# Kernel optimization log

Measured on AMD Instinct MI355X. Metric: run time of the kernel, lower is better.

The kernel has to match this reference:

```python
import jax, jax.numpy as jnp
import numpy as np

N = 20000      # nodes
E = 320000     # edges (before self-loops)
IN, HID, H, OUT = 256, 64, 8, 16
NEG_SLOPE = 0.2  # PyG GATConv default


def _gat_layer(x, src, dst, W, a_src, a_dst, b, heads, ch, concat):
    """One PyG-style GATConv (eval mode, self-loops already in src/dst).
    x: [N, F_in]; W: [F_in, heads*ch]; a_src/a_dst: [heads, ch]; b: bias."""
    n = x.shape[0]
    h = (x @ W).reshape(n, heads, ch)                      # [N, H, C]
    alpha_src = jnp.sum(h * a_src, axis=-1)                # [N, H]
    alpha_dst = jnp.sum(h * a_dst, axis=-1)                # [N, H]
    e = jax.nn.leaky_relu(alpha_src[src] + alpha_dst[dst], NEG_SLOPE)  # [Et, H]
    # segment softmax over incoming edges of each dst node (numerically stable)
    m = jax.ops.segment_max(e, dst, num_segments=n)
    m = jnp.where(jnp.isfinite(m), m, 0.0)
    ex = jnp.exp(e - m[dst])
    denom = jax.ops.segment_sum(ex, dst, num_segments=n)
    alpha = ex / jnp.maximum(denom[dst], 1e-16)            # [Et, H]
    # message = alpha * h[src], scatter-add to dst
    out = jax.ops.segment_sum(alpha[:, :, None] * h[src], dst, num_segments=n)  # [N,H,C]
    out = out.reshape(n, heads * ch) if concat else out.mean(axis=1)
    return out + b


def setup_inputs() -> dict:
    key = jax.random.key(0)
    ks = jax.random.split(key, 16)
    p = lambda k, shape, fan: (jax.random.normal(k, shape, jnp.float32) / np.float32(np.sqrt(fan)))
    return {
        "x": jax.random.normal(ks[0], (N, IN), jnp.float32),
        "edge_index": jax.random.randint(ks[1], (2, E), 0, N, dtype=jnp.int32),
        "W1": p(ks[2], (IN, H * HID), IN),
        "a_src1": p(ks[3], (H, HID), HID), "a_dst1": p(ks[4], (H, HID), HID),
        "b1": jnp.zeros((H * HID,), jnp.float32),
        "W2": p(ks[5], (H * HID, H * HID), H * HID),
        "a_src2": p(ks[6], (H, HID), HID), "a_dst2": p(ks[7], (H, HID), HID),
        "b2": jnp.zeros((H * HID,), jnp.float32),
        "W3": p(ks[8], (H * HID, OUT), H * HID),
        "a_src3": p(ks[9], (1, OUT), OUT), "a_dst3": p(ks[10], (1, OUT), OUT),
        "b3": jnp.zeros((OUT,), jnp.float32),
    }


def reference(x, edge_index, W1, a_src1, a_dst1, b1, W2, a_src2, a_dst2, b2,
              W3, a_src3, a_dst3, b3):
    # add self-loops once (PyG GATConv default add_self_loops=True)
    loops = jnp.arange(N, dtype=edge_index.dtype)
    src = jnp.concatenate([edge_index[0], loops])
    dst = jnp.concatenate([edge_index[1], loops])
    h = _gat_layer(x, src, dst, W1, a_src1, a_dst1, b1, H, HID, True)
    h = jax.nn.elu(h)
    h = _gat_layer(h, src, dst, W2, a_src2, a_dst2, b2, H, HID, True)
    h = jax.nn.elu(h)
    h = _gat_layer(h, src, dst, W3, a_src3, a_dst3, b3, 1, OUT, False)
    return jax.nn.log_softmax(h, axis=1)
```

## Files before the change

### kernel.cpp

```cpp
#include <hip/hip_runtime.h>
#include <hip/hip_fp8.h>

#define NEG_SLOPE 0.2f

typedef _Float16 f16x8 __attribute__((ext_vector_type(8)));
typedef float f32x4 __attribute__((ext_vector_type(4)));
typedef float f32x2 __attribute__((ext_vector_type(2)));

#if defined(__has_builtin)
#if __has_builtin(__builtin_amdgcn_cvt_pk_f32_fp8)
#define HAVE_PK_FP8 1
#endif
#endif

__device__ __forceinline__ float lrelu(float x){ return x >= 0.0f ? x : NEG_SLOPE * x; }
__device__ __forceinline__ float elu1(float x){ return x > 0.0f ? x : __expf(x) - 1.0f; }

__device__ __forceinline__ void gload_lds16(const _Float16* g, _Float16* l){
  __builtin_amdgcn_global_load_lds(
      (const __attribute__((address_space(1))) unsigned int*)g,
      (__attribute__((address_space(3))) unsigned int*)l, 16, 0, 0);
}

__device__ __forceinline__ float f8_to_f32(unsigned char b){
  __hip_fp8_e4m3 t; t.__x = (__hip_fp8_storage_t)b; return (float)t;
}

__device__ __forceinline__ void dq8(uint2 u, float* f){
#ifdef HAVE_PK_FP8
  f32x2 a = __builtin_amdgcn_cvt_pk_f32_fp8(u.x, false);
  f32x2 b = __builtin_amdgcn_cvt_pk_f32_fp8(u.x, true);
  f32x2 c = __builtin_amdgcn_cvt_pk_f32_fp8(u.y, false);
  f32x2 d = __builtin_amdgcn_cvt_pk_f32_fp8(u.y, true);
  f[0]=a[0]; f[1]=a[1]; f[2]=b[0]; f[3]=b[1];
  f[4]=c[0]; f[5]=c[1]; f[6]=d[0]; f[7]=d[1];
#else
  const unsigned char* p = (const unsigned char*)&u;
  #pragma unroll
  for (int j = 0; j < 8; ++j) f[j] = f8_to_f32(p[j]);
#endif
}

union H8U { uint4 u; _Float16 h[8]; };

__global__ __launch_bounds__(256) void prep_kernel(
    const float* __restrict__ x, _Float16* __restrict__ x16, int cvtb, int valid, int total,
    const float* __restrict__ W1, _Float16* __restrict__ W1T,
    const float* __restrict__ W2, _Float16* __restrict__ W2T,
    const int* __restrict__ dstp, int E, int N, int* __restrict__ counts)
{
  __shared__ float tile[32][33];
  int b = blockIdx.x;
  const int tid = threadIdx.x;
  if (b < cvtb){
    int i = (b * 256 + tid) * 8;
    if (i < total){
      H8U o;
      if (i + 8 <= valid){
        float4 v0 = *(const float4*)(x + i);
        float4 v1 = *(const float4*)(x + i + 4);
        o.h[0] = (_Float16)v0.x; o.h[1] = (_Float16)v0.y; o.h[2] = (_Float16)v0.z; o.h[3] = (_Float16)v0.w;
        o.h[4] = (_Float16)v1.x; o.h[5] = (_Float16)v1.y; o.h[6] = (_Float16)v1.z; o.h[7] = (_Float16)v1.w;
      } else {
        #pragma unroll
        for (int j = 0; j < 8; ++j) o.h[j] = (i + j < valid) ? (_Float16)x[i + j] : (_Float16)0.0f;
      }
      *(uint4*)(x16 + i) = o.u;
    }
    return;
  }
  b -= cvtb;
  if (b < 128 + 256){
    const float* W; _Float16* WT; int K, Nn, bb;
    if (b < 128){ W = W1; WT = W1T; K = 256; Nn = 512; bb = b; }
    else        { W = W2; WT = W2T; K = 512; Nn = 512; bb = b - 128; }
    const int nbk = K / 32;
    const int k0 = (bb % nbk) * 32, n0 = (bb / nbk) * 32;
    const int tx = tid & 31, ty = tid >> 5;
    for (int i = ty; i < 32; i += 8)
      tile[i][tx] = W[(size_t)(k0 + i) * Nn + n0 + tx];
    __syncthreads();
    for (int i = ty; i < 32; i += 8)
      WT[(size_t)(n0 + i) * K + k0 + tx] = (_Float16)tile[tx][i];
    return;
  }
  b -= 384;
  {
    int i = b * 256 + tid;
    if (i < E + N){
      int d = (i < E) ? dstp[i] : (i - E);
      atomicAdd(&counts[d], 1);
    }
  }
}

__global__ __launch_bounds__(256) void block_sum_kernel(const int* __restrict__ counts, int N, int* __restrict__ bsum){
  __shared__ int ws[4];
  const int lane = threadIdx.x & 63, wave = threadIdx.x >> 6;
  int i = blockIdx.x * 256 + threadIdx.x;
  int v = (i < N) ? counts[i] : 0;
  #pragma unroll
  for (int msk = 1; msk < 64; msk <<= 1) v += __shfl_xor(v, msk);
  if (lane == 0) ws[wave] = v;
  __syncthreads();
  if (threadIdx.x == 0) bsum[blockIdx.x] = ws[0] + ws[1] + ws[2] + ws[3];
}

__global__ __launch_bounds__(256) void scan_bsum_kernel(int* __restrict__ bsum, int nb, int* __restrict__ offsets, int N){
  __shared__ int tmp[256];
  const int t = threadIdx.x;
  int v = (t < nb) ? bsum[t] : 0;
  tmp[t] = v;
  __syncthreads();
  #pragma unroll
  for (int ofs = 1; ofs < 256; ofs <<= 1){
    int add = (t >= ofs) ? tmp[t - ofs] : 0;
    __syncthreads();
    tmp[t] += add;
    __syncthreads();
  }
  if (t < nb) bsum[t] = tmp[t] - v;
  if (t == nb - 1) offsets[N] = tmp[t];
}

__global__ __launch_bounds__(256) void scan_within_kernel(const int* __restrict__ counts, const int* __restrict__ bsum,
                                                          int* __restrict__ offsets, int N){
  __shared__ int wsum[4];
  const int lane = threadIdx.x & 63, wave = threadIdx.x >> 6;
  int i = blockIdx.x * 256 + threadIdx.x;
  int v = (i < N) ? counts[i] : 0;
  int sc = v;
  #pragma unroll
  for (int ofs = 1; ofs < 64; ofs <<= 1){
    int t = __shfl_up(sc, ofs);
    if (lane >= ofs) sc += t;
  }
  if (lane == 63) wsum[wave] = sc;
  __syncthreads();
  int woff = 0;
  #pragma unroll
  for (int w = 0; w < 4; ++w) if (w < wave) woff += wsum[w];
  if (i < N) offsets[i] = bsum[blockIdx.x] + woff + sc - v;
}

__global__ void fill_kernel(const int* __restrict__ src, const int* __restrict__ dst, int E, int N,
                            const int* __restrict__ offsets, int* __restrict__ cursor, int* __restrict__ csr_src){
  int i = blockIdx.x * blockDim.x + threadIdx.x;
  if (i < E + N){
    int s, d;
    if (i < E){ s = src[i]; d = dst[i]; } else { s = i - E; d = i - E; }
    int pos = atomicAdd(&cursor[d], 1);
    csr_src[offsets[d] + pos] = s;
  }
}

__global__ __launch_bounds__(256) void gemm_f16_mfma_q(
    const _Float16* __restrict__ A, const _Float16* __restrict__ BT,
    unsigned char* __restrict__ H8, float* __restrict__ SC,
    const float* __restrict__ a_src, const float* __restrict__ a_dst,
    float* __restrict__ AS, float* __restrict__ AD,
    int M, int Nn, int K)
{
  __shared__ _Float16 As[128 * 64];
  __shared__ _Float16 Bs[128 * 64];
  const int tid = threadIdx.x;
  const int lane = tid & 63;
  const int wave = tid >> 6;
  const int wr = wave >> 1, wc = wave & 1;
  const int row0 = blockIdx.x * 128;
  const int col0 = blockIdx.y * 128;
  const int r15 = lane & 15;
  const int kgrp = lane >> 4;
  const int head = 2 * blockIdx.y + wc;

  f32x4 acc[4][4];
  #pragma unroll
  for (int m = 0; m < 4; ++m)
    #pragma unroll
    for (int n = 0; n < 4; ++n)
      acc[m][n] = (f32x4){0.f, 0.f, 0.f, 0.f};

  for (int k0 = 0; k0 < K; k0 += 64){
    #pragma unroll
    for (int it = 0; it < 4; ++it){
      int idx = it * 2048 + tid * 8;
      int r = idx >> 6, c = idx & 63;
      gload_lds16(A  + (size_t)(row0 + r) * K + k0 + c, &As[idx]);
      gload_lds16(BT + (size_t)(col0 + r) * K + k0 + c, &Bs[idx]);
    }
    __syncthreads();
    #pragma unroll
    for (int kk = 0; kk < 2; ++kk){
      const int cc = kk * 32 + kgrp * 8;
      f16x8 av[4], bv[4];
      #pragma unroll
      for (int q = 0; q < 4; ++q){
        av[q] = *(const f16x8*)&As[(wr * 64 + q * 16 + r15) * 64 + cc];
        bv[q] = *(const f16x8*)&Bs[(wc * 64 + q * 16 + r15) * 64 + cc];
      }
      #pragma unroll
      for (int m = 0; m < 4; ++m)
        #pragma unroll
        for (int n = 0; n < 4; ++n)
          acc[m][n] = __builtin_amdgcn_mfma_f32_16x16x32_f16(av[m], bv[n], acc[m][n], 0, 0, 0);
    }
    __syncthreads();
  }

  float asv[4], adv[4];
  #pragma unroll
  for (int n = 0; n < 4; ++n){
    asv[n] = a_src[head * 64 + n * 16 + r15];
    adv[n] = a_dst[head * 64 + n * 16 + r15];
  }
  #pragma unroll
  for (int m = 0; m < 4; ++m){
    #pragma unroll
    for (int j = 0; j < 4; ++j){
      float ps = 0.f, pd = 0.f;
      #pragma unroll
      for (int n = 0; n < 4; ++n){
        float c = acc[m][n][j];
        ps += c * asv[n];
        pd += c * adv[n];
      }
      #pragma unroll
      for (int msk = 1; msk < 16; msk <<= 1){
        ps += __shfl_xor(ps, msk);
        pd += __shfl_xor(pd, msk);
      }
      int row = row0 + wr * 64 + m * 16 + kgrp * 4 + j;
      if (r15 == 0 && row < M){
        AS[(size_t)row * 8 + head] = ps;
        AD[(size_t)row * 8 + head] = pd;
      }
    }
  }

  unsigned char* stg = reinterpret_cast<unsigned char*>(As) + wave * 4096;
  #pragma unroll
  for (int m = 0; m < 4; ++m){
    #pragma unroll
    for (int j = 0; j < 4; ++j){
      float a = fmaxf(fmaxf(fabsf(acc[m][0][j]), fabsf(acc[m][1][j])),
                      fmaxf(fabsf(acc[m][2][j]), fabsf(acc[m][3][j])));
      #pragma unroll
      for (int msk = 1; msk < 16; msk <<= 1) a = fmaxf(a, __shfl_xor(a, msk));
      float inv = (a > 1e-30f) ? (448.0f / a) : 0.0f;
      int rm = m * 16 + kgrp * 4 + j;
      #pragma unroll
      for (int n = 0; n < 4; ++n){
        __hip_fp8_e4m3 q(acc[m][n][j] * inv);
        stg[rm * 64 + n * 16 + r15] = (unsigned char)q.__x;
      }
      if (r15 == 0){
        int row = row0 + wr * 64 + rm;
        SC[(size_t)row * 8 + head] = a * (1.0f / 448.0f);
      }
    }
  }
  #pragma unroll
  for (int it = 0; it < 4; ++it){
    int srow = it * 16 + (lane >> 2);
    int chunk = lane & 3;
    uint4 v = *reinterpret_cast<const uint4*>(stg + srow * 64 + chunk * 16);
    int row = row0 + wr * 64 + srow;
    *reinterpret_cast<uint4*>(H8 + (size_t)row * 512 + head * 64 + chunk * 16) = v;
  }
}

__global__ __launch_bounds__(128) void agg_f8(
    const unsigned char* __restrict__ H8, const float* __restrict__ SC,
    const float* __restrict__ AS, const float* __restrict__ AD,
    const int* __restrict__ offsets, const int* __restrict__ csr_src,
    const float* __restrict__ bias, _Float16* __restrict__ O16, int N)
{
  const int wave = threadIdx.x >> 6, lane = threadIdx.x & 63;
  const int d = blockIdx.x * 2 + wave;
  if (d >= N) return;
  const int beg = offsets[d], end = offsets[d + 1];
  const int h8 = lane & 7;
  const int hA = lane >> 3;
  const float adv = AD[(size_t)d * 8 + h8];

  float m = -1e30f;
  for (int sl = beg + hA; sl < end; sl += 8){
    int s = csr_src[sl];
    m = fmaxf(m, lrelu(AS[(size_t)s * 8 + h8] + adv));
  }
  #pragma unroll
  for (int msk = 8; msk < 64; msk <<= 1) m = fmaxf(m, __shfl_xor(m, msk));
  const float mH = __shfl(m, hA);
  const float aH = __shfl(adv, hA);

  float acc[8];
  #pragma unroll
  for (int j = 0; j < 8; ++j) acc[j] = 0.f;
  float den = 0.f;
  const unsigned char* Hb = H8 + lane * 8;
  int slot = beg;
  for (; slot + 4 <= end; slot += 4){
    int   s[4]; float p[4], c[4]; uint2 u[4];
    #pragma unroll
    for (int q = 0; q < 4; ++q) s[q] = csr_src[slot + q];
    #pragma unroll
    for (int q = 0; q < 4; ++q){ p[q] = AS[(size_t)s[q] * 8 + hA]; c[q] = SC[(size_t)s[q] * 8 + hA]; }
    #pragma unroll
    for (int q = 0; q < 4; ++q) u[q] = *(const uint2*)(Hb + (size_t)s[q] * 512);
    #pragma unroll
    for (int q = 0; q < 4; ++q){
      float e = __expf(lrelu(p[q] + aH) - mH);
      den += e;
      float w = e * c[q];
      float f[8];
      dq8(u[q], f);
      #pragma unroll
      for (int j = 0; j < 8; ++j) acc[j] += w * f[j];
    }
  }
  for (; slot < end; ++slot){
    int s0 = csr_src[slot];
    float p0 = AS[(size_t)s0 * 8 + hA];
    float c0 = SC[(size_t)s0 * 8 + hA];
    uint2 u0 = *(const uint2*)(Hb + (size_t)s0 * 512);
    float e = __expf(lrelu(p0 + aH) - mH);
    den += e;
    float w = e * c0;
    float f[8];
    dq8(u0, f);
    #pragma unroll
    for (int j = 0; j < 8; ++j) acc[j] += w * f[j];
  }

  const float di = 1.0f / fmaxf(den, 1e-16f);
  const float4 b0 = *(const float4*)(bias + lane * 8);
  const float4 b1 = *(const float4*)(bias + lane * 8 + 4);
  float bb[8] = {b0.x, b0.y, b0.z, b0.w, b1.x, b1.y, b1.z, b1.w};
  H8U O;
  #pragma unroll
  for (int j = 0; j < 8; ++j) O.h[j] = (_Float16)elu1(acc[j] * di + bb[j]);
  *(uint4*)(O16 + (size_t)d * 512 + lane * 8) = O.u;
}

__global__ __launch_bounds__(256) void gemm_n16_f16(const _Float16* __restrict__ X, const float* __restrict__ W,
                                                    float* __restrict__ Y,
                                                    const float* __restrict__ a3s, const float* __restrict__ a3d,
                                                    float* __restrict__ AS3, float* __restrict__ AD3,
                                                    int M, int K){
  __shared__ float Ws[512 * 16];
  __shared__ float Xs[64][68];
  const int tid = threadIdx.x;
  for (int i = tid; i < K * 16; i += 256) Ws[i] = W[i];
  const int tx = tid & 15;
  const int ty = tid >> 4;
  const int row0 = blockIdx.x * 64;
  float acc[4] = {0.f, 0.f, 0.f, 0.f};
  for (int k0 = 0; k0 < K; k0 += 64){
    __syncthreads();
    #pragma unroll
    for (int it = 0; it < 2; ++it){
      int idx = it * 2048 + tid * 8;
      int r = idx >> 6, c = idx & 63;
      H8U U; U.u = *(const uint4*)(X + (size_t)(row0 + r) * K + k0 + c);
      float4 f0 = make_float4((float)U.h[0], (float)U.h[1], (float)U.h[2], (float)U.h[3]);
      float4 f1 = make_float4((float)U.h[4], (float)U.h[5], (float)U.h[6], (float)U.h[7]);
      *(float4*)&Xs[r][c] = f0;
      *(float4*)&Xs[r][c + 4] = f1;
    }
    __syncthreads();
    #pragma unroll
    for (int kk = 0; kk < 64; ++kk){
      float w = Ws[(k0 + kk) * 16 + tx];
      #pragma unroll
      for (int i = 0; i < 4; ++i) acc[i] += Xs[ty * 4 + i][kk] * w;
    }
  }
  const float sc = a3s[tx], dc = a3d[tx];
  #pragma unroll
  for (int i = 0; i < 4; ++i){
    int grow = row0 + ty * 4 + i;
    if (grow < M) Y[(size_t)grow * 16 + tx] = acc[i];
    float ps = acc[i] * sc, pd = acc[i] * dc;
    #pragma unroll
    for (int msk = 1; msk < 16; msk <<= 1){
      ps += __shfl_xor(ps, msk);
      pd += __shfl_xor(pd, msk);
    }
    if (tx == 0 && grow < M){ AS3[grow] = ps; AD3[grow] = pd; }
  }
}

__global__ __launch_bounds__(256) void agg3_kernel(
    const float* __restrict__ H3,
    const float* __restrict__ AS3, const float* __restrict__ AD3,
    const int* __restrict__ offsets, const int* __restrict__ csr_src,
    const float* __restrict__ bias, float* __restrict__ Out, int N)
{
  const int wave = threadIdx.x >> 6, lane = threadIdx.x & 63;
  const int d = blockIdx.x * 4 + wave;
  if (d >= N) return;
  const int beg = offsets[d], end = offsets[d + 1];
  const float adv = AD3[d];
  float m = -1e30f;
  for (int slot = beg + lane; slot < end; slot += 64){
    int s = csr_src[slot];
    m = fmaxf(m, lrelu(AS3[s] + adv));
  }
  #pragma unroll
  for (int msk = 1; msk < 64; msk <<= 1) m = fmaxf(m, __shfl_xor(m, msk));

  const int c = lane & 15;
  float acc = 0.f, den = 0.f;
  for (int slot = beg + (lane >> 4); slot < end; slot += 4){
    int s = csr_src[slot];
    float e = __expf(lrelu(AS3[s] + adv) - m);
    den += e;
    acc += e * H3[(size_t)s * 16 + c];
  }
  acc += __shfl_xor(acc, 16);
  acc += __shfl_xor(acc, 32);
  den += __shfl_xor(den, 16);
  den += __shfl_xor(den, 32);
  float v = acc / fmaxf(den, 1e-16f) + bias[c];
  float mm = v;
  #pragma unroll
  for (int msk = 1; msk < 16; msk <<= 1) mm = fmaxf(mm, __shfl_xor(mm, msk));
  float se = __expf(v - mm);
  #pragma unroll
  for (int msk = 1; msk < 16; msk <<= 1) se += __shfl_xor(se, msk);
  float r = v - mm - __logf(se);
  if (lane < 16) Out[(size_t)d * 16 + lane] = r;
}

extern "C" void kernel_launch(void* const* d_in, const int* in_sizes, int n_in,
                              void* d_out, int out_size, void* d_ws, size_t ws_size,
                              hipStream_t stream)
{
  const float* x   = (const float*)d_in[0];
  const int*   ei  = (const int*)d_in[1];
  const float* W1  = (const float*)d_in[2];
  const float* as1 = (const float*)d_in[3];
  const float* ad1 = (const float*)d_in[4];
  const float* b1  = (const float*)d_in[5];
  const float* W2  = (const float*)d_in[6];
  const float* as2 = (const float*)d_in[7];
  const float* ad2 = (const float*)d_in[8];
  const float* b2  = (const float*)d_in[9];
  const float* W3  = (const float*)d_in[10];
  const float* as3 = (const float*)d_in[11];
  const float* ad3 = (const float*)d_in[12];
  const float* b3  = (const float*)d_in[13];

  const int N    = in_sizes[0] / 256;
  const int E    = in_sizes[1] / 2;
  const int Et   = E + N;
  const int Mpad = (N + 127) & ~127;
  const int nb   = (N + 255) / 256;
  const int* src = ei;
  const int* dst = ei + E;

  char* base = (char*)d_ws;
  size_t off = 0;
  auto take = [&](size_t bytes) -> char* {
    char* p = base + off;
    off = (off + bytes + 255) & ~(size_t)255;
    return p;
  };
  _Float16* x16  = (_Float16*)take((size_t)Mpad * 256 * 2);
  _Float16* O16  = (_Float16*)take((size_t)Mpad * 512 * 2);
  unsigned char* H8 = (unsigned char*)take((size_t)Mpad * 512);
  float* SC   = (float*)take((size_t)Mpad * 8 * 4);
  _Float16* W1T  = (_Float16*)take((size_t)512 * 256 * 2);
  _Float16* W2T  = (_Float16*)take((size_t)512 * 512 * 2);
  float* AS   = (float*)take((size_t)N * 8 * 4);
  float* AD   = (float*)take((size_t)N * 8 * 4);
  float* H3   = (float*)take((size_t)N * 16 * 4);
  float* AS3  = (float*)take((size_t)N * 4);
  float* AD3  = (float*)take((size_t)N * 4);
  int* counts  = (int*)take((size_t)2 * N * 4);
  int* cursor  = counts + N;
  int* offsets = (int*)take((size_t)(N + 1) * 4);
  int* bsum    = (int*)take((size_t)(nb + 1) * 4);
  int* csr     = (int*)take((size_t)Et * 4);
  if (off > ws_size) return;

  hipMemsetAsync(counts, 0, (size_t)2 * N * 4, stream);
  const int tb = 256;
  const int cvtb = Mpad / 8;
  const int cntb = (Et + tb - 1) / tb;
  prep_kernel<<<cvtb + 384 + cntb, tb, 0, stream>>>(
      x, x16, cvtb, N * 256, Mpad * 256, W1, W1T, W2, W2T, dst, E, N, counts);
  block_sum_kernel<<<nb, 256, 0, stream>>>(counts, N, bsum);
  scan_bsum_kernel<<<1, 256, 0, stream>>>(bsum, nb, offsets, N);
  scan_within_kernel<<<nb, 256, 0, stream>>>(counts, bsum, offsets, N);
  fill_kernel<<<(Et + tb - 1) / tb, tb, 0, stream>>>(src, dst, E, N, offsets, cursor, csr);

  const int gM = Mpad / 128;
  gemm_f16_mfma_q<<<dim3(gM, 4), 256, 0, stream>>>(x16, W1T, H8, SC, as1, ad1, AS, AD, N, 512, 256);
  agg_f8<<<(N + 1) / 2, 128, 0, stream>>>(H8, SC, AS, AD, offsets, csr, b1, O16, N);
  gemm_f16_mfma_q<<<dim3(gM, 4), 256, 0, stream>>>(O16, W2T, H8, SC, as2, ad2, AS, AD, N, 512, 512);
  agg_f8<<<(N + 1) / 2, 128, 0, stream>>>(H8, SC, AS, AD, offsets, csr, b2, O16, N);
  gemm_n16_f16<<<(N + 63) / 64, 256, 0, stream>>>(O16, W3, H3, as3, ad3, AS3, AD3, N, 512);
  agg3_kernel<<<(N + 3) / 4, 256, 0, stream>>>(H3, AS3, AD3, offsets, csr, b3, (float*)d_out, N);
}
```

Measured before the change: 237.9 us.

## Permute FP8 feature layout to drop LDS staging in GEMM epilogue

The GEMM epilogue now packs each lane's four quantized values into one 32-bit word with a packed fp32-to-fp8 convert. It writes that word straight to global memory in a permuted column order, replacing the byte-wise LDS staging and the 16-byte copy-out. The aggregation kernel's output store is rewritten to undo the permutation, so it now writes pairs of halves at strided offsets instead of one 16-byte vector per lane. This removes LDS traffic and per-byte conversions. The cost is narrower global stores in both kernels.

```diff
diff --git a/kernel.cpp b/kernel.cpp
--- a/kernel.cpp
+++ b/kernel.cpp
@@ -9,7 +9,10 @@
 
 #if defined(__has_builtin)
 #if __has_builtin(__builtin_amdgcn_cvt_pk_f32_fp8)
-#define HAVE_PK_FP8 1
+#define HAVE_PK_F32_FP8 1
+#endif
+#if __has_builtin(__builtin_amdgcn_cvt_pk_fp8_f32)
+#define HAVE_PK_FP8_F32 1
 #endif
 #endif
 
@@ -27,7 +30,7 @@
 }
 
 __device__ __forceinline__ void dq8(uint2 u, float* f){
-#ifdef HAVE_PK_FP8
+#ifdef HAVE_PK_F32_FP8
   f32x2 a = __builtin_amdgcn_cvt_pk_f32_fp8(u.x, false);
   f32x2 b = __builtin_amdgcn_cvt_pk_f32_fp8(u.x, true);
   f32x2 c = __builtin_amdgcn_cvt_pk_f32_fp8(u.y, false);
@@ -41,7 +44,20 @@
 #endif
 }
 
+__device__ __forceinline__ unsigned int pack4_fp8(float v0, float v1, float v2, float v3){
+#ifdef HAVE_PK_FP8_F32
+  int pk = __builtin_amdgcn_cvt_pk_fp8_f32(v0, v1, 0, false);
+  pk = __builtin_amdgcn_cvt_pk_fp8_f32(v2, v3, pk, true);
+  return (unsigned int)pk;
+#else
+  __hip_fp8_e4m3 q0(v0), q1(v1), q2(v2), q3(v3);
+  return (unsigned int)q0.__x | ((unsigned int)q1.__x << 8) |
+         ((unsigned int)q2.__x << 16) | ((unsigned int)q3.__x << 24);
+#endif
+}
+
 union H8U { uint4 u; _Float16 h[8]; };
+union P2U { _Float16 h[2]; unsigned int u; };
 
 __global__ __launch_bounds__(256) void prep_kernel(
     const float* __restrict__ x, _Float16* __restrict__ x16, int cvtb, int valid, int total,
@@ -237,7 +253,6 @@
     }
   }
 
-  unsigned char* stg = reinterpret_cast<unsigned char*>(As) + wave * 4096;
   #pragma unroll
   for (int m = 0; m < 4; ++m){
     #pragma unroll
@@ -247,25 +262,12 @@
       #pragma unroll
       for (int msk = 1; msk < 16; msk <<= 1) a = fmaxf(a, __shfl_xor(a, msk));
       float inv = (a > 1e-30f) ? (448.0f / a) : 0.0f;
-      int rm = m * 16 + kgrp * 4 + j;
-      #pragma unroll
-      for (int n = 0; n < 4; ++n){
-        __hip_fp8_e4m3 q(acc[m][n][j] * inv);
-        stg[rm * 64 + n * 16 + r15] = (unsigned char)q.__x;
-      }
-      if (r15 == 0){
-        int row = row0 + wr * 64 + rm;
-        SC[(size_t)row * 8 + head] = a * (1.0f / 448.0f);
-      }
-    }
-  }
-  #pragma unroll
-  for (int it = 0; it < 4; ++it){
-    int srow = it * 16 + (lane >> 2);
-    int chunk = lane & 3;
-    uint4 v = *reinterpret_cast<const uint4*>(stg + srow * 64 + chunk * 16);
-    int row = row0 + wr * 64 + srow;
-    *reinterpret_cast<uint4*>(H8 + (size_t)row * 512 + head * 64 + chunk * 16) = v;
+      int row = row0 + wr * 64 + m * 16 + kgrp * 4 + j;
+      unsigned int pk = pack4_fp8(acc[m][0][j] * inv, acc[m][1][j] * inv,
+                                  acc[m][2][j] * inv, acc[m][3][j] * inv);
+      *(unsigned int*)(H8 + (size_t)row * 512 + head * 64 + r15 * 4) = pk;
+      if (r15 == 0) SC[(size_t)row * 8 + head] = a * (1.0f / 448.0f);
+    }
   }
 }
 
@@ -281,6 +283,7 @@
   const int beg = offsets[d], end = offsets[d + 1];
   const int h8 = lane & 7;
   const int hA = lane >> 3;
+  const int l3 = lane & 7;
   const float adv = AD[(size_t)d * 8 + h8];
 
   float m = -1e30f;
@@ -333,13 +336,16 @@
   }
 
   const float di = 1.0f / fmaxf(den, 1e-16f);
-  const float4 b0 = *(const float4*)(bias + lane * 8);
-  const float4 b1 = *(const float4*)(bias + lane * 8 + 4);
-  float bb[8] = {b0.x, b0.y, b0.z, b0.w, b1.x, b1.y, b1.z, b1.w};
-  H8U O;
-  #pragma unroll
-  for (int j = 0; j < 8; ++j) O.h[j] = (_Float16)elu1(acc[j] * di + bb[j]);
-  *(uint4*)(O16 + (size_t)d * 512 + lane * 8) = O.u;
+  _Float16* Ob = O16 + (size_t)d * 512 + hA * 64 + 2 * l3;
+  const float* Bb = bias + hA * 64 + 2 * l3;
+  #pragma unroll
+  for (int j = 0; j < 4; ++j){
+    float2 bv = *(const float2*)(Bb + j * 16);
+    P2U P;
+    P.h[0] = (_Float16)elu1(acc[j] * di + bv.x);
+    P.h[1] = (_Float16)elu1(acc[j + 4] * di + bv.y);
+    *(unsigned int*)(Ob + j * 16) = P.u;
+  }
 }
 
 __global__ __launch_bounds__(256) void gemm_n16_f16(const _Float16* __restrict__ X, const float* __restrict__ W,
```

Result: no change. 236.8 us (-0.5%).
